# Kernel tuning notes

Hardware: AMD Instinct MI355X
Metric: run time of the kernel (lower is better)

Reference implementation:

```python
import jax, jax.numpy as jnp
import numpy as np

N, C, T, V = 64, 64, 64, 25   # batch, channels, frames, joints
S, W = 8, 3                   # num_subset, window_size
IC = C // S                   # inter_channels = out_channels // num_subset = 8
OC = 64                       # out_channels
EPS = 1e-5


def setup_inputs() -> dict:
    key = jax.random.key(0)
    ks = jax.random.split(key, 24)
    std = 0.05
    x = jax.random.normal(ks[0], (N, C, V, T), jnp.float32)
    # fixed skeleton graphs (buffers, non-trainable)
    graph = (jax.random.uniform(ks[1], (S, V, V)) > 0.7).astype(jnp.float32)
    graph = jnp.clip(graph + jnp.eye(V, dtype=jnp.float32)[None], 0.0, 1.0)
    graph_a = jax.random.uniform(ks[2], (V, V), jnp.float32) / V
    # conv1x1 weights (out, in) + biases
    in_w = jax.random.normal(ks[3], (S * IC, C), jnp.float32) * std
    in_b = jax.random.normal(ks[4], (S * IC,), jnp.float32) * 0.01
    inup_w = jax.random.normal(ks[5], (S * IC, C), jnp.float32) * std
    inup_b = jax.random.normal(ks[6], (S * IC,), jnp.float32) * 0.01
    diff_w = jax.random.normal(ks[7], (C, C), jnp.float32) * std
    diff_b = jax.random.normal(ks[8], (C,), jnp.float32) * 0.01
    att0 = jnp.ones((1, S, W * V, V), jnp.float32) / V  # attention0s
    out_w = jax.random.normal(ks[9], (OC, S * C), jnp.float32) * std
    out_b = jax.random.normal(ks[10], (OC,), jnp.float32) * 0.01
    out_gamma = jnp.ones((OC,), jnp.float32)
    out_beta = jnp.zeros((OC,), jnp.float32)
    out_rm = jax.random.normal(ks[11], (OC,), jnp.float32) * 0.01
    out_rv = jnp.ones((OC,), jnp.float32)
    ff_w = jax.random.normal(ks[12], (OC, OC), jnp.float32) * std
    ff_b = jax.random.normal(ks[13], (OC,), jnp.float32) * 0.01
    ff_gamma = jnp.ones((OC,), jnp.float32)
    ff_beta = jnp.zeros((OC,), jnp.float32)
    ff_rm = jax.random.normal(ks[14], (OC,), jnp.float32) * 0.01
    ff_rv = jnp.ones((OC,), jnp.float32)
    return dict(x=x, graph=graph, graph_a=graph_a, in_w=in_w, in_b=in_b,
                inup_w=inup_w, inup_b=inup_b, diff_w=diff_w, diff_b=diff_b,
                att0=att0, out_w=out_w, out_b=out_b, out_gamma=out_gamma,
                out_beta=out_beta, out_rm=out_rm, out_rv=out_rv, ff_w=ff_w,
                ff_b=ff_b, ff_gamma=ff_gamma, ff_beta=ff_beta, ff_rm=ff_rm,
                ff_rv=ff_rv)


def _bn(x, g, b, m, v):  # inference-mode BatchNorm2d over channel dim 1
    scale = (g / jnp.sqrt(v + EPS))[None, :, None, None]
    return x * scale + (b - m * g / jnp.sqrt(v + EPS))[None, :, None, None]


def _leaky(x):
    return jnp.where(x > 0, x, 0.1 * x)


def _forward(x, graph, graph_a, in_w, in_b, inup_w, inup_b, diff_w, diff_b,
             att0, out_w, out_b, out_gamma, out_beta, out_rm, out_rv,
             ff_w, ff_b, ff_gamma, ff_beta, ff_rm, ff_rv):
    xp = jnp.transpose(x, (0, 1, 3, 2))          # (N,C,T,V)
    identity = xp
    # temporal window unfold: (N,C,T,W*V)
    xpad = jnp.pad(xp, ((0, 0), (0, 0), (1, 1), (0, 0)))
    upf = jnp.stack([xpad[:, :, w:w + T, :] for w in range(W)], axis=3)
    upf = upf.reshape(N, C, T, W * V)
    # q/k projections (conv1x1)
    k = (jnp.einsum('nctv,oc->notv', xp, in_w) + in_b[None, :, None, None])
    k = k.reshape(N, S, IC, T, V)
    q = (jnp.einsum('nctu,oc->notu', upf, inup_w) + inup_b[None, :, None, None])
    q = q.reshape(N, S, IC, T, W * V)
    att = jnp.einsum('nsctu,nsctv->nsuv', q, k) / (IC * T)  # (N,S,WV,V)
    # per-subset adjacency mask (graph[i] tiled over window rows)
    mask = jnp.tile(graph, (1, W, 1)) > 0                    # (S,WV,V)
    att = jnp.where(mask[None], att, jnp.float32(-9e15))
    att = jax.nn.softmax(att, axis=-1)
    # diff gate
    d = jnp.einsum('nctu,uv->nctv', xp, graph_a)
    d = jnp.einsum('nctv,oc->notv', d, diff_w) + diff_b[None, :, None, None]
    d = jnp.tile(d, (1, 1, 1, W)) - upf                      # (N,C,T,WV)
    d = d.reshape(N, S, C // S, T, W, V)
    gate = jax.nn.sigmoid(d.mean(axis=(2, 3, 5)))            # (N,S,W)
    att = att * jnp.tile(gate[..., None], (1, 1, V, 1))      # (N,S,WV,1) tiled
    att = att + att0
    # aggregate
    y = jnp.einsum('nctu,nsuv->nsctv', upf, att).reshape(N, S * C, T, V)
    y = _bn(jnp.einsum('nctv,oc->notv', y, out_w) + out_b[None, :, None, None],
            out_gamma, out_beta, out_rm, out_rv)
    y = _leaky(xp + y)                                       # downs1 = identity
    y = _bn(jnp.einsum('nctv,oc->notv', y, ff_w) + ff_b[None, :, None, None],
            ff_gamma, ff_beta, ff_rm, ff_rv)
    y = _leaky(xp + y)                                       # downs2 = identity
    z = jax.nn.relu(y + identity)
    return jnp.transpose(z, (0, 1, 3, 2))                    # back to (N,C,V,T)


def reference(x, graph, graph_a, in_w, in_b, inup_w, inup_b, diff_w, diff_b,
              att0, out_w, out_b, out_gamma, out_beta, out_rm, out_rv,
              ff_w, ff_b, ff_gamma, ff_beta, ff_rm, ff_rv):
    return _forward(x, graph, graph_a, in_w, in_b, inup_w, inup_b, diff_w,
                    diff_b, att0, out_w, out_b, out_gamma, out_beta, out_rm,
                    out_rv, ff_w, ff_b, ff_gamma, ff_beta, ff_rm, ff_rv)
```

## Files before the change

### kernel.cpp

```cpp
#include <hip/hip_runtime.h>
#include <hip/hip_bf16.h>
#include <math.h>

#define Nn 64
#define Cn 64
#define Tn 64
#define Vn 25
#define Sn 8
#define ICn 8
#define Wn 3
#define WVn 75

typedef __attribute__((ext_vector_type(8))) short s16x8;
typedef __attribute__((ext_vector_type(4))) short s16x4;
typedef __attribute__((ext_vector_type(4))) float f32x4;

#define MFMA16(a, b, c) __builtin_amdgcn_mfma_f32_16x16x32_bf16(a, b, c, 0, 0, 0)

static __device__ inline unsigned short f2bf(float f) {
    __hip_bfloat16 h = __float2bfloat16(f);
    return *reinterpret_cast<unsigned short*>(&h);
}
static __device__ inline float bf2f(unsigned short u) {
    union { unsigned int i; float f; } x;
    x.i = ((unsigned int)u) << 16;
    return x.f;
}

__global__ __launch_bounds__(64) void k_red(const float* __restrict__ x,
                                            const float* __restrict__ ga,
                                            const float* __restrict__ ow,
                                            const float* __restrict__ fw,
                                            float* __restrict__ red,
                                            unsigned short* __restrict__ owb,
                                            unsigned short* __restrict__ fwb) {
    const int c = blockIdx.x, n = blockIdx.y;
    const int lane = threadIdx.x;
    if (n == 0) {
        for (int j = lane; j < 512; j += 64) owb[c * 512 + j] = f2bf(ow[c * 512 + j]);
        fwb[c * 64 + lane] = f2bf(fw[c * 64 + lane]);
    }
    float rs = 0.f, r0 = 0.f, r63 = 0.f, xg = 0.f;
    if (lane < Vn) {
        const float* row = x + ((size_t)(n * Cn + c) * Vn + lane) * Tn;
        float g = 0.f;
        for (int j = 0; j < Vn; ++j) g += ga[lane * Vn + j];
        for (int t = 0; t < Tn; ++t) rs += row[t];
        r0 = row[0];
        r63 = row[Tn - 1];
        xg = rs * g;
    }
    for (int off = 32; off > 0; off >>= 1) {
        rs += __shfl_down(rs, off);
        r0 += __shfl_down(r0, off);
        r63 += __shfl_down(r63, off);
        xg += __shfl_down(xg, off);
    }
    if (lane == 0) {
        float* p = red + (size_t)(n * Cn + c) * 4;
        p[0] = rs; p[1] = r0; p[2] = r63; p[3] = xg;
    }
}

__global__ __launch_bounds__(256) void k_proj2(
    const float* __restrict__ x,
    const float* __restrict__ in_w, const float* __restrict__ in_b,
    const float* __restrict__ inup_w, const float* __restrict__ inup_b,
    unsigned short* __restrict__ pk, unsigned short* __restrict__ pq) {
    const int n = blockIdx.x, v = blockIdx.y;
    const int tid = threadIdx.x;
    const int lane = tid & 63, wv = tid >> 6;
    const int r16 = lane & 15, g4 = lane >> 4;

    __shared__ unsigned short WL[128 * 64];
    __shared__ unsigned short XT[64 * 64];
    __shared__ unsigned short CL[64 * 128];
    __shared__ float bias[128];

    if (tid < 128) bias[tid] = (tid < 64) ? in_b[tid] : inup_b[tid - 64];

    for (int idx = tid; idx < 2048; idx += 256) {
        const int o2 = idx >> 4, c4 = idx & 15;
        const float4 d = (o2 < 64)
            ? *(const float4*)(in_w + o2 * 64 + c4 * 4)
            : *(const float4*)(inup_w + (o2 - 64) * 64 + c4 * 4);
        s16x4 p;
        p[0] = (short)f2bf(d.x); p[1] = (short)f2bf(d.y);
        p[2] = (short)f2bf(d.z); p[3] = (short)f2bf(d.w);
        const int ch = c4 >> 1;
        *(s16x4*)&WL[o2 * 64 + (((ch ^ (o2 & 7))) << 3) + (c4 & 1) * 4] = p;
    }
    for (int idx = tid; idx < 1024; idx += 256) {
        const int c = idx >> 4, t4 = idx & 15;
        const float4 d = *(const float4*)(x +
            ((size_t)((n * Cn + c) * Vn + v)) * Tn + t4 * 4);
        const float dv[4] = {d.x, d.y, d.z, d.w};
#pragma unroll
        for (int jj = 0; jj < 4; ++jj) {
            const int t = t4 * 4 + jj;
            XT[t * 64 + (((c >> 3) ^ (t & 7)) << 3) + (c & 7)] = f2bf(dv[jj]);
        }
    }
    __syncthreads();

#pragma unroll
    for (int mi = 0; mi < 2; ++mi) {
        const int mt = wv * 2 + mi;
        const int o2r = mt * 16 + r16;
#pragma unroll
        for (int nt2 = 0; nt2 < 4; ++nt2) {
            const int t = nt2 * 16 + r16;
            f32x4 acc = (f32x4){0.f, 0.f, 0.f, 0.f};
#pragma unroll
            for (int ks = 0; ks < 2; ++ks) {
                const int ch = ks * 4 + g4;
                const s16x8 a = *(const s16x8*)&WL[o2r * 64 + ((ch ^ (o2r & 7)) << 3)];
                const s16x8 b = *(const s16x8*)&XT[t * 64 + ((ch ^ (t & 7)) << 3)];
                acc = MFMA16(a, b, acc);
            }
            const int tcol = nt2 * 16 + r16;
            const int ob = mt * 16 + g4 * 4;
            s16x4 p;
#pragma unroll
            for (int r = 0; r < 4; ++r) p[r] = f2bf(acc[r] + bias[ob + r]);
            const int ch = ob >> 3;
            *(s16x4*)&CL[tcol * 128 + ((ch ^ (tcol & 7)) << 3) + (ob & 7)] = p;
        }
    }
    __syncthreads();

    for (int j = tid; j < 1024; j += 256) {
        const int p = j & 15, t = j >> 4;
        const s16x8 d = *(const s16x8*)&CL[t * 128 + ((p ^ (t & 7)) << 3)];
        const int po = p & 7;
        unsigned short* dst = (p < 8) ? pk : pq;
        *(s16x8*)(dst + (((size_t)(n * Vn + v) * Tn + t) << 6) + po * 8) = d;
    }
}

__global__ __launch_bounds__(256) void k_att3(
    const unsigned short* __restrict__ pq, const unsigned short* __restrict__ pk,
    const float* __restrict__ inup_b, const float* __restrict__ graph,
    const float* __restrict__ att0, const float* __restrict__ red,
    const float* __restrict__ diff_w, const float* __restrict__ diff_b,
    unsigned short* __restrict__ attB) {
    const int n = blockIdx.x, s = blockIdx.y;
    const int tid = threadIdx.x;
    const int lane = tid & 63, wv = tid >> 6;
    const int r16 = lane & 15, g4 = lane >> 4;

    __shared__ unsigned short QS[25 * 536];
    __shared__ unsigned short KS[32 * 512];
    __shared__ float attL[80 * 33];
    __shared__ float gp4[8][4];
    __shared__ float g3[3];

    if (tid < 8) {
        const int oc = s * ICn + tid;
        float a = 0.f;
        for (int c = 0; c < Cn; ++c)
            a += red[(n * Cn + c) * 4 + 3] * diff_w[oc * Cn + c];
        gp4[tid][0] = a + 1600.f * diff_b[oc];
        gp4[tid][1] = red[(n * Cn + oc) * 4 + 0];
        gp4[tid][2] = red[(n * Cn + oc) * 4 + 1];
        gp4[tid][3] = red[(n * Cn + oc) * 4 + 2];
    }
    for (int i = tid; i < 2048; i += 256) {
        const int t = i & 63, v = i >> 6;
        s16x8 d = (s16x8){0, 0, 0, 0, 0, 0, 0, 0};
        if (v < Vn)
            d = *(const s16x8*)(pk + (((size_t)(n * Vn + v) * Tn + t) << 6) + s * ICn);
        *(s16x8*)&KS[v * 512 + ((t ^ (v & 7)) << 3)] = d;
    }
    for (int i = tid; i < 1600; i += 256) {
        const int t = i & 63, uu = i >> 6;
        const s16x8 d = *(const s16x8*)(pq +
            (((size_t)(n * Vn + uu) * Tn + t) << 6) + s * ICn);
        *(s16x8*)&QS[uu * 536 + (t + 1) * 8] = d;
    }
    if (tid < 50) {
        const int uu = tid >> 1, slot = (tid & 1) * 65;
#pragma unroll
        for (int cc = 0; cc < ICn; ++cc)
            QS[uu * 536 + slot * 8 + cc] = f2bf(inup_b[s * ICn + cc]);
    }
    __syncthreads();

    for (int tile = wv; tile < 10; tile += 4) {
        const int mt = tile >> 1, nt = tile & 1;
        const int u = mt * 16 + r16;
        const int w = u / 25, uu = u % 25;
        const int v = nt * 16 + r16;
        const unsigned short* qbase = &QS[uu * 536 + (g4 + w) * 8];
        const unsigned short* kbase = &KS[v * 512];
        f32x4 acc = (f32x4){0.f, 0.f, 0.f, 0.f};
#pragma unroll
        for (int kb = 0; kb < 16; ++kb) {
            const s16x8 af = *(const s16x8*)(qbase + kb * 32);
            const s16x8 bf = *(const s16x8*)(kbase + (((kb * 4 + g4) ^ (v & 7)) << 3));
            acc = MFMA16(af, bf, acc);
        }
#pragma unroll
        for (int r = 0; r < 4; ++r)
            attL[(mt * 16 + g4 * 4 + r) * 33 + v] = acc[r];
    }
    if (tid == 0) {
        float sumd2 = 0.f, rsum = 0.f, rr0 = 0.f, rr63 = 0.f;
#pragma unroll
        for (int cc = 0; cc < 8; ++cc) {
            sumd2 += gp4[cc][0]; rsum += gp4[cc][1];
            rr0 += gp4[cc][2]; rr63 += gp4[cc][3];
        }
        const float inv = 1.f / 12800.f;
        g3[0] = 1.f / (1.f + expf(-(sumd2 - (rsum - rr63)) * inv));
        g3[1] = 1.f / (1.f + expf(-(sumd2 - rsum) * inv));
        g3[2] = 1.f / (1.f + expf(-(sumd2 - (rsum - rr0)) * inv));
    }
    __syncthreads();

    if (tid < WVn) {
        const int u = tid, u0 = u % Vn;
        const float* gr = graph + (s * Vn + u0) * Vn;
        float av[Vn];
        float mx = -1e30f;
#pragma unroll
        for (int v = 0; v < Vn; ++v) {
            float a = attL[u * 33 + v] * (1.f / 512.f);
            av[v] = (gr[v] > 0.f) ? a : -1e30f;
            mx = fmaxf(mx, av[v]);
        }
        float ssum = 0.f;
#pragma unroll
        for (int v = 0; v < Vn; ++v) {
            float e = (av[v] > -1e29f) ? expf(av[v] - mx) : 0.f;
            av[v] = e;
            ssum += e;
        }
        const float sc = g3[u % Wn] / ssum;
        const float* a0 = att0 + (s * WVn + u) * Vn;
#pragma unroll
        for (int v = 0; v < Vn; ++v) attL[u * 33 + v] = av[v] * sc + a0[v];
    }
    __syncthreads();

    unsigned short* ab = attB + ((size_t)(n * Sn + s)) * 32 * 96;
    for (int i = tid; i < 32 * 96; i += 256) {
        const int v = i / 96, kk = i % 96;
        const int w2 = kk >> 5, vp = kk & 31;
        float val = (v < Vn && vp < Vn) ? attL[(w2 * Vn + vp) * 33 + v] : 0.f;
        ab[i] = f2bf(val);
    }
}

__global__ __launch_bounds__(256) void k_trans(const float* __restrict__ x,
                                               unsigned short* __restrict__ xT) {
    const int n = blockIdx.x, cb = blockIdx.y;
    const int c0 = cb * 4;
    const int tid = threadIdx.x;
    __shared__ unsigned short XL[4][25][66];

    for (int i = tid; i < 1600; i += 256) {
        const int piece = i & 15, row = i >> 4;
        const int cl = row / 25, v = row - cl * 25;
        const float4 d = *(const float4*)(x +
            ((size_t)((n * Cn + c0 + cl) * Vn + v)) * Tn + piece * 4);
        unsigned short* dst = &XL[cl][v][piece * 4];
        dst[0] = f2bf(d.x); dst[1] = f2bf(d.y); dst[2] = f2bf(d.z); dst[3] = f2bf(d.w);
    }
    __syncthreads();
    for (int j = tid; j < 1024; j += 256) {
        const int p = j & 3, cl = (j >> 2) & 3, t = j >> 4;
        const int v0 = (p ^ cl) * 8;
        unsigned short buf[8];
#pragma unroll
        for (int jj = 0; jj < 8; ++jj) {
            const int v = v0 + jj;
            buf[jj] = (v < Vn) ? XL[cl][v][t] : (unsigned short)0;
        }
        *(s16x8*)(xT + ((size_t)(n * Tn + t) * 2048) + (c0 + cl) * 32 + p * 8) =
            *(const s16x8*)buf;
    }
}

__global__ __launch_bounds__(256, 3) void k_main7(
    const unsigned short* __restrict__ xT, const unsigned short* __restrict__ attB,
    const unsigned short* __restrict__ out_wbf, const float* __restrict__ out_b,
    const float* __restrict__ og, const float* __restrict__ obeta,
    const float* __restrict__ orm, const float* __restrict__ orv,
    const unsigned short* __restrict__ ff_wbf, const float* __restrict__ ff_b,
    const float* __restrict__ fg, const float* __restrict__ fbeta,
    const float* __restrict__ frm, const float* __restrict__ frv,
    float* __restrict__ out) {
    const int n = blockIdx.x, t = blockIdx.y;
    const int tid = threadIdx.x;
    const int lane = tid & 63, wv = tid >> 6;
    const int r16 = lane & 15, g4 = lane >> 4;

    __shared__ unsigned short xs3[3 * 2048];
    __shared__ unsigned short y2L[32 * 512];
    __shared__ unsigned short y1L[32 * 64];
    __shared__ float bnp[384];

    if (tid < 64) {
        int o = tid;
        float so = og[o] * rsqrtf(orv[o] + 1e-5f);
        bnp[o] = so; bnp[64 + o] = obeta[o] - orm[o] * so; bnp[128 + o] = out_b[o];
        float sf = fg[o] * rsqrtf(frv[o] + 1e-5f);
        bnp[192 + o] = sf; bnp[256 + o] = fbeta[o] - frm[o] * sf; bnp[320 + o] = ff_b[o];
    }
    for (int ch = tid; ch < 768; ch += 256) {
        const int kb = ch >> 8, off = ch & 255;
        const int tg = t - 1 + kb;
        s16x8 d = (s16x8){0, 0, 0, 0, 0, 0, 0, 0};
        if (tg >= 0 && tg < Tn)
            d = *(const s16x8*)(xT + ((size_t)(n * Tn + tg) * 2048) + off * 8);
        *(s16x8*)&xs3[ch * 8] = d;
    }
    __syncthreads();

    s16x8 af[4][3];
#pragma unroll
    for (int m = 0; m < 4; ++m) {
        const int c = m * 16 + r16;
#pragma unroll
        for (int kb = 0; kb < 3; ++kb)
            af[m][kb] = *(const s16x8*)&xs3[kb * 2048 + c * 32 + ((g4 ^ (c & 3)) << 3)];
    }
#pragma unroll
    for (int si = 0; si < 2; ++si) {
        const int s = wv * 2 + si;
        const unsigned short* aB = attB + ((size_t)(n * Sn + s)) * 32 * 96;
        s16x8 bfr[3][2];
#pragma unroll
        for (int k = 0; k < 3; ++k)
#pragma unroll
            for (int nt = 0; nt < 2; ++nt)
                bfr[k][nt] = *(const s16x8*)(aB + (nt * 16 + r16) * 96 + k * 32 + g4 * 8);
#pragma unroll
        for (int m = 0; m < 4; ++m) {
            f32x4 c0 = (f32x4){0.f, 0.f, 0.f, 0.f};
            f32x4 c1 = (f32x4){0.f, 0.f, 0.f, 0.f};
#pragma unroll
            for (int kb = 0; kb < 3; ++kb) {
                c0 = MFMA16(af[m][kb], bfr[kb][0], c0);
                c1 = MFMA16(af[m][kb], bfr[kb][1], c1);
            }
            const int cw = m * 16 + g4 * 4;
            s16x4 p0, p1;
#pragma unroll
            for (int r = 0; r < 4; ++r) { p0[r] = f2bf(c0[r]); p1[r] = f2bf(c1[r]); }
            const int v0 = r16, v1 = 16 + r16;
            *(s16x4*)&y2L[v0 * 512 + (s * 8 + ((cw >> 3) ^ (v0 & 7))) * 8 + (cw & 7)] = p0;
            *(s16x4*)&y2L[v1 * 512 + (s * 8 + ((cw >> 3) ^ (v1 & 7))) * 8 + (cw & 7)] = p1;
        }
    }
    __syncthreads();

    f32x4 accO[2];
    accO[0] = (f32x4){0.f, 0.f, 0.f, 0.f};
    accO[1] = (f32x4){0.f, 0.f, 0.f, 0.f};
    const int orow = wv * 16 + r16;
#pragma unroll
    for (int ks = 0; ks < 16; ++ks) {
        const s16x8 wa = *(const s16x8*)(out_wbf + (size_t)orow * 512 + ks * 32 + g4 * 8);
        const int cidx = ks * 4 + g4;
        const int srow = cidx >> 3, lc = cidx & 7;
#pragma unroll
        for (int na = 0; na < 2; ++na) {
            const int v = na * 16 + r16;
            const s16x8 b = *(const s16x8*)&y2L[v * 512 + (srow * 8 + (lc ^ (v & 7))) * 8];
            accO[na] = MFMA16(wa, b, accO[na]);
        }
    }
    float xvc[2][4];
    const int ob = wv * 16 + g4 * 4;
#pragma unroll
    for (int na = 0; na < 2; ++na) {
        const int v = na * 16 + r16;
        s16x4 p;
#pragma unroll
        for (int r = 0; r < 4; ++r) {
            const int o = ob + r;
            const float xv = bf2f(xs3[2048 + o * 32 + ((((v >> 3)) ^ (o & 3)) << 3) + (v & 7)]);
            xvc[na][r] = xv;
            float val = (accO[na][r] + bnp[128 + o]) * bnp[o] + bnp[64 + o];
            float y1 = xv + val;
            y1 = (y1 > 0.f) ? y1 : 0.1f * y1;
            p[r] = f2bf(y1);
        }
        *(s16x4*)&y1L[v * 64 + (((ob >> 3) ^ (v & 7)) << 3) + (ob & 7)] = p;
    }
    __syncthreads();

    f32x4 accF[2];
    accF[0] = (f32x4){0.f, 0.f, 0.f, 0.f};
    accF[1] = (f32x4){0.f, 0.f, 0.f, 0.f};
#pragma unroll
    for (int ks = 0; ks < 2; ++ks) {
        const s16x8 fa = *(const s16x8*)(ff_wbf + (size_t)orow * 64 + ks * 32 + g4 * 8);
        const int cidx = ks * 4 + g4;
#pragma unroll
        for (int na = 0; na < 2; ++na) {
            const int v = na * 16 + r16;
            const s16x8 b = *(const s16x8*)&y1L[v * 64 + ((cidx ^ (v & 7)) << 3)];
            accF[na] = MFMA16(fa, b, accF[na]);
        }
    }
#pragma unroll
    for (int na = 0; na < 2; ++na) {
        const int v = na * 16 + r16;
        if (v < Vn) {
#pragma unroll
            for (int r = 0; r < 4; ++r) {
                const int o = ob + r;
                const float xv = xvc[na][r];
                float val = (accF[na][r] + bnp[320 + o]) * bnp[192 + o] + bnp[256 + o];
                float y2v = xv + val;
                y2v = (y2v > 0.f) ? y2v : 0.1f * y2v;
                float outv = y2v + xv;
                outv = (outv > 0.f) ? outv : 0.f;
                out[((size_t)(n * Cn + o) * Vn + v) * Tn + t] = outv;
            }
        }
    }
}

extern "C" void kernel_launch(void* const* d_in, const int* in_sizes, int n_in,
                              void* d_out, int out_size, void* d_ws, size_t ws_size,
                              hipStream_t stream) {
    const float* x       = (const float*)d_in[0];
    const float* graph   = (const float*)d_in[1];
    const float* graph_a = (const float*)d_in[2];
    const float* in_w    = (const float*)d_in[3];
    const float* in_b    = (const float*)d_in[4];
    const float* inup_w  = (const float*)d_in[5];
    const float* inup_b  = (const float*)d_in[6];
    const float* diff_w  = (const float*)d_in[7];
    const float* diff_b  = (const float*)d_in[8];
    const float* att0    = (const float*)d_in[9];
    const float* out_w   = (const float*)d_in[10];
    const float* out_b   = (const float*)d_in[11];
    const float* og      = (const float*)d_in[12];
    const float* obeta   = (const float*)d_in[13];
    const float* orm     = (const float*)d_in[14];
    const float* orv     = (const float*)d_in[15];
    const float* ff_w    = (const float*)d_in[16];
    const float* ff_b    = (const float*)d_in[17];
    const float* fg      = (const float*)d_in[18];
    const float* fbeta   = (const float*)d_in[19];
    const float* frm     = (const float*)d_in[20];
    const float* frv     = (const float*)d_in[21];
    float* out = (float*)d_out;

    char* wsb = (char*)d_ws;
    float* red_ws  = (float*)(wsb);
    unsigned short* attB = (unsigned short*)(wsb + 71680);
    unsigned short* owb  = (unsigned short*)(wsb + 3217408);
    unsigned short* fwb  = (unsigned short*)(wsb + 3282944);
    unsigned short* pq = (unsigned short*)(wsb + 3291136);
    unsigned short* pk = (unsigned short*)(wsb + 16398336);
    unsigned short* xT = (unsigned short*)(wsb + 3291136);

    k_red<<<dim3(Cn, Nn), 64, 0, stream>>>(x, graph_a, out_w, ff_w, red_ws, owb, fwb);
    k_proj2<<<dim3(Nn, Vn), 256, 0, stream>>>(x, in_w, in_b, inup_w, inup_b, pk, pq);
    k_att3<<<dim3(Nn, Sn), 256, 0, stream>>>(pq, pk, inup_b, graph, att0,
                                             red_ws, diff_w, diff_b, attB);
    k_trans<<<dim3(Nn, 16), 256, 0, stream>>>(x, xT);
    k_main7<<<dim3(Nn, Tn), 256, 0, stream>>>(xT, attB, owb, out_b, og, obeta,
                                              orm, orv, fwb, ff_b, fg, fbeta,
                                              frm, frv, out);
}
```

Before: 127.0 us.

## Pre-swizzle weights, attention and projections into MFMA fragment order for coalesced loads

Stores the bf16 out/ff weights and the attention matrices in per-lane MFMA fragment order, so the main kernel fetches each fragment with one contiguous 16-byte load per lane (lane*8). It also changes the pq/pk projection layout to per-subset slabs, so the attention kernel reads contiguous 8-channel rows instead of strided ones. The goal is to cut uncoalesced global traffic in the hot main and attention kernels. In exchange, the one-time conversion kernels do more index arithmetic and scattered reads when writing these layouts.

```diff
diff --git a/kernel.cpp b/kernel.cpp
--- a/kernel.cpp
+++ b/kernel.cpp
@@ -37,8 +37,18 @@
     const int c = blockIdx.x, n = blockIdx.y;
     const int lane = threadIdx.x;
     if (n == 0) {
-        for (int j = lane; j < 512; j += 64) owb[c * 512 + j] = f2bf(ow[c * 512 + j]);
-        fwb[c * 64 + lane] = f2bf(fw[c * 64 + lane]);
+        for (int j8 = 0; j8 < 8; ++j8) {
+            const int q = c * 512 + j8 * 64 + lane;
+            const int j = q & 7, ln = (q >> 3) & 63, fi = q >> 9;
+            const int wvq = fi >> 4, ksq = fi & 15;
+            owb[q] = f2bf(ow[(wvq * 16 + (ln & 15)) * 512 + ksq * 32 + (ln >> 4) * 8 + j]);
+        }
+        {
+            const int q = c * 64 + lane;
+            const int j = q & 7, ln = (q >> 3) & 63, fi = q >> 9;
+            const int wvq = fi >> 1, ksq = fi & 1;
+            fwb[q] = f2bf(fw[(wvq * 16 + (ln & 15)) * 64 + ksq * 32 + (ln >> 4) * 8 + j]);
+        }
     }
     float rs = 0.f, r0 = 0.f, r63 = 0.f, xg = 0.f;
     if (lane < Vn) {
@@ -129,12 +139,12 @@
     }
     __syncthreads();
 
-    for (int j = tid; j < 1024; j += 256) {
-        const int p = j & 15, t = j >> 4;
+    for (int jj = tid; jj < 1024; jj += 256) {
+        const int t = jj & 63, p = jj >> 6;
         const s16x8 d = *(const s16x8*)&CL[t * 128 + ((p ^ (t & 7)) << 3)];
-        const int po = p & 7;
+        const int s8 = p & 7;
         unsigned short* dst = (p < 8) ? pk : pq;
-        *(s16x8*)(dst + (((size_t)(n * Vn + v) * Tn + t) << 6) + po * 8) = d;
+        *(s16x8*)(dst + ((((size_t)(n * Sn + s8) * Vn + v) * Tn + t) << 3)) = d;
     }
 }
 
@@ -169,13 +179,13 @@
         const int t = i & 63, v = i >> 6;
         s16x8 d = (s16x8){0, 0, 0, 0, 0, 0, 0, 0};
         if (v < Vn)
-            d = *(const s16x8*)(pk + (((size_t)(n * Vn + v) * Tn + t) << 6) + s * ICn);
+            d = *(const s16x8*)(pk + ((((size_t)(n * Sn + s) * Vn + v) * Tn + t) << 3));
         *(s16x8*)&KS[v * 512 + ((t ^ (v & 7)) << 3)] = d;
     }
     for (int i = tid; i < 1600; i += 256) {
         const int t = i & 63, uu = i >> 6;
         const s16x8 d = *(const s16x8*)(pq +
-            (((size_t)(n * Vn + uu) * Tn + t) << 6) + s * ICn);
+            ((((size_t)(n * Sn + s) * Vn + uu) * Tn + t) << 3));
         *(s16x8*)&QS[uu * 536 + (t + 1) * 8] = d;
     }
     if (tid < 50) {
@@ -243,12 +253,14 @@
     }
     __syncthreads();
 
-    unsigned short* ab = attB + ((size_t)(n * Sn + s)) * 32 * 96;
-    for (int i = tid; i < 32 * 96; i += 256) {
-        const int v = i / 96, kk = i % 96;
-        const int w2 = kk >> 5, vp = kk & 31;
-        float val = (v < Vn && vp < Vn) ? attL[(w2 * Vn + vp) * 33 + v] : 0.f;
-        ab[i] = f2bf(val);
+    unsigned short* ab = attB + ((size_t)(n * Sn + s)) * 3072;
+    for (int idx = tid; idx < 3072; idx += 256) {
+        const int j = idx & 7, ln = (idx >> 3) & 63, f = idx >> 9;
+        const int k = f >> 1, nt = f & 1;
+        const int v = nt * 16 + (ln & 15);
+        const int vp = (ln >> 4) * 8 + j;
+        float val = (v < Vn && vp < Vn) ? attL[(k * Vn + vp) * 33 + v] : 0.f;
+        ab[idx] = f2bf(val);
     }
 }
 
@@ -282,7 +294,7 @@
     }
 }
 
-__global__ __launch_bounds__(256, 3) void k_main7(
+__global__ __launch_bounds__(256, 3) void k_main11(
     const unsigned short* __restrict__ xT, const unsigned short* __restrict__ attB,
     const unsigned short* __restrict__ out_wbf, const float* __restrict__ out_b,
     const float* __restrict__ og, const float* __restrict__ obeta,
@@ -329,13 +341,13 @@
 #pragma unroll
     for (int si = 0; si < 2; ++si) {
         const int s = wv * 2 + si;
-        const unsigned short* aB = attB + ((size_t)(n * Sn + s)) * 32 * 96;
+        const unsigned short* aB = attB + ((size_t)(n * Sn + s)) * 3072;
         s16x8 bfr[3][2];
 #pragma unroll
         for (int k = 0; k < 3; ++k)
 #pragma unroll
             for (int nt = 0; nt < 2; ++nt)
-                bfr[k][nt] = *(const s16x8*)(aB + (nt * 16 + r16) * 96 + k * 32 + g4 * 8);
+                bfr[k][nt] = *(const s16x8*)(aB + (((k * 2 + nt) * 64 + lane) << 3));
 #pragma unroll
         for (int m = 0; m < 4; ++m) {
             f32x4 c0 = (f32x4){0.f, 0.f, 0.f, 0.f};
@@ -359,10 +371,10 @@
     f32x4 accO[2];
     accO[0] = (f32x4){0.f, 0.f, 0.f, 0.f};
     accO[1] = (f32x4){0.f, 0.f, 0.f, 0.f};
-    const int orow = wv * 16 + r16;
 #pragma unroll
     for (int ks = 0; ks < 16; ++ks) {
-        const s16x8 wa = *(const s16x8*)(out_wbf + (size_t)orow * 512 + ks * 32 + g4 * 8);
+        const s16x8 wa = *(const s16x8*)(out_wbf +
+            ((((size_t)(wv * 16 + ks)) * 64 + lane) << 3));
         const int cidx = ks * 4 + g4;
         const int srow = cidx >> 3, lc = cidx & 7;
 #pragma unroll
@@ -397,7 +409,7 @@
     accF[1] = (f32x4){0.f, 0.f, 0.f, 0.f};
 #pragma unroll
     for (int ks = 0; ks < 2; ++ks) {
-        const s16x8 fa = *(const s16x8*)(ff_wbf + (size_t)orow * 64 + ks * 32 + g4 * 8);
+        const s16x8 fa = *(const s16x8*)(ff_wbf + (((wv * 2 + ks) * 64 + lane) << 3));
         const int cidx = ks * 4 + g4;
 #pragma unroll
         for (int na = 0; na < 2; ++na) {
@@ -466,7 +478,7 @@
     k_att3<<<dim3(Nn, Sn), 256, 0, stream>>>(pq, pk, inup_b, graph, att0,
                                              red_ws, diff_w, diff_b, attB);
     k_trans<<<dim3(Nn, 16), 256, 0, stream>>>(x, xT);
-    k_main7<<<dim3(Nn, Tn), 256, 0, stream>>>(xT, attB, owb, out_b, og, obeta,
-                                              orm, orv, fwb, ff_b, fg, fbeta,
-                                              frm, frv, out);
-}
+    k_main11<<<dim3(Nn, Tn), 256, 0, stream>>>(xT, attB, owb, out_b, og, obeta,
+                                               orm, orv, fwb, ff_b, fg, fbeta,
+                                               frm, frv, out);
+}
```

New measurement: 107.7 us. 1.18x faster.
